# Optimization experiments

Hardware: AMD Instinct MI355X
Metric: run time of the kernel (lower is better)

## Reference

```python
import jax, jax.numpy as jnp
import numpy as np

N_HEADS = 16

def setup_inputs() -> dict:
    key = jax.random.key(0)
    ks = jax.random.split(key, 4)
    B, T, C = 2, 2048, 1024
    scale = 0.02
    return {
        "x": jax.random.normal(ks[0], (B, T, C), dtype=jnp.float32),
        "w_qkv": jax.random.normal(ks[1], (C, 3 * C), dtype=jnp.float32) * scale,
        "b_qkv": jnp.zeros((3 * C,), dtype=jnp.float32),
        "w_out": jax.random.normal(ks[2], (C, C), dtype=jnp.float32) * scale,
        "b_out": jnp.zeros((C,), dtype=jnp.float32),
    }

def reference(x, w_qkv, b_qkv, w_out, b_out):
    B, T, C = x.shape
    H = N_HEADS
    hd = C // H
    qkv = x @ w_qkv + b_qkv                      # [B,T,3C]
    q, k, v = jnp.split(qkv, 3, axis=-1)
    # [B,H,T,hd]
    q = q.reshape(B, T, H, hd).transpose(0, 2, 1, 3)
    k = k.reshape(B, T, H, hd).transpose(0, 2, 1, 3)
    v = v.reshape(B, T, H, hd).transpose(0, 2, 1, 3)
    att = jnp.einsum('bhqd,bhkd->bhqk', q, k) / jnp.sqrt(jnp.float32(hd))
    causal = jnp.tril(jnp.ones((T, T), dtype=bool))
    att = jnp.where(causal, att, -jnp.inf)
    att = jax.nn.softmax(att, axis=-1)
    # dropout is identity in eval mode (p effectively 0 for reference)
    y = jnp.einsum('bhqk,bhkd->bhqd', att, v)
    y = y.transpose(0, 2, 1, 3).reshape(B, T, C)
    return y @ w_out + b_out
```

## Files before the change

### kernel.cpp

```cpp
#include <hip/hip_runtime.h>
#include <hip/hip_bf16.h>

#define DEVI __device__ __forceinline__

typedef __attribute__((ext_vector_type(8))) short bf16x8_t;
typedef __attribute__((ext_vector_type(4))) float f32x4_t;
typedef __attribute__((ext_vector_type(4))) short s16x4_t;
typedef __attribute__((ext_vector_type(2))) unsigned int u32x2_t;

#define QSCALE 0.18033688011112043f
#define EXP2F(x) __builtin_amdgcn_exp2f(x)

static DEVI unsigned short f2b_bits(float f) {
    unsigned int u = __float_as_uint(f);
    unsigned int r = (u + 0x7fffu + ((u >> 16) & 1u)) >> 16;
    return (unsigned short)r;
}

static DEVI unsigned int cvtpk_bf16(float lo, float hi) {
    unsigned int r;
    asm("v_cvt_pk_bf16_f32 %0, %1, %2" : "=v"(r) : "v"(lo), "v"(hi));
    return r;
}

static DEVI void gload16(const short* g, short* l) {
    __builtin_amdgcn_global_load_lds((const __attribute__((address_space(1))) void*)g,
                                     (__attribute__((address_space(3))) void*)l, 16, 0, 0);
}

__global__ void cast_bf16_k(const float* __restrict__ in, short* __restrict__ out, long n) {
    long i = ((long)blockIdx.x * blockDim.x + threadIdx.x) * 4;
    if (i >= n) return;
    const float4 v = *(const float4*)(in + i);
    s16x4_t o;
    o[0] = (short)f2b_bits(v.x); o[1] = (short)f2b_bits(v.y);
    o[2] = (short)f2b_bits(v.z); o[3] = (short)f2b_bits(v.w);
    *(s16x4_t*)(out + i) = o;
}

__global__ void transpose_cast(const float* __restrict__ w, short* __restrict__ wT,
                               int K, int N) {
    __shared__ float tile[32][33];
    const int n0 = blockIdx.x * 32, k0 = blockIdx.y * 32;
    const int tx = threadIdx.x, ty = threadIdx.y;
#pragma unroll
    for (int i = 0; i < 4; ++i)
        tile[ty + 8 * i][tx] = w[(long)(k0 + ty + 8 * i) * N + n0 + tx];
    __syncthreads();
#pragma unroll
    for (int i = 0; i < 4; ++i)
        wT[(long)(n0 + ty + 8 * i) * K + k0 + tx] = (short)f2b_bits(tile[tx][ty + 8 * i]);
}

template<int MODE>
__global__ __launch_bounds__(256, 2) void gemm_bt(const short* __restrict__ A,
                                                  const short* __restrict__ Bt,
                                                  const float* __restrict__ bias,
                                                  void* __restrict__ Cv,
                                                  short* __restrict__ vtp,
                                                  int M, int N, int K) {
    __shared__ __align__(16) short lsA[2][128 * 32];
    __shared__ __align__(16) short lsB[2][128 * 32];
    const int tid = threadIdx.x;
    const int lane = tid & 63;
    const int w = tid >> 6;
    const int wr = w >> 1, wc = w & 1;
    const int l15 = lane & 15, lg = lane >> 4;
    const long m0 = (long)blockIdx.y * 128;
    const long n0 = (long)blockIdx.x * 128;

    f32x4_t acc[4][4] = {};

    const int srow = tid >> 2;
    const int scol = (tid & 3) * 8;
    const short* gA = A + (m0 + srow) * (long)K + scol;
    const short* gB = Bt + (n0 + srow) * (long)K + scol;

    auto STAGE = [&](int kt, int bi) {
        gload16(gA + kt,                &lsA[bi][tid * 8]);
        gload16(gA + kt + (long)64 * K, &lsA[bi][tid * 8 + 2048]);
        gload16(gB + kt,                &lsB[bi][tid * 8]);
        gload16(gB + kt + (long)64 * K, &lsB[bi][tid * 8 + 2048]);
    };

    const int nt = K >> 5;
    STAGE(0, 0);
    __syncthreads();
    int buf = 0;

    for (int i = 0; i < nt; ++i) {
        if (i + 1 < nt) STAGE((i + 1) << 5, buf ^ 1);
        bf16x8_t af[4], bfr[4];
#pragma unroll
        for (int m = 0; m < 4; ++m)
            af[m] = *(const bf16x8_t*)&lsA[buf][(wr * 64 + m * 16 + l15) * 32 + lg * 8];
#pragma unroll
        for (int n = 0; n < 4; ++n)
            bfr[n] = *(const bf16x8_t*)&lsB[buf][(wc * 64 + n * 16 + l15) * 32 + lg * 8];
        __builtin_amdgcn_s_setprio(1);
#pragma unroll
        for (int m = 0; m < 4; ++m)
#pragma unroll
            for (int n = 0; n < 4; ++n)
                acc[m][n] = __builtin_amdgcn_mfma_f32_16x16x32_bf16(af[m], bfr[n], acc[m][n], 0, 0, 0);
        __builtin_amdgcn_s_setprio(0);
        __syncthreads();
        buf ^= 1;
    }

#pragma unroll
    for (int n = 0; n < 4; ++n) {
        const int col = (int)n0 + wc * 64 + n * 16 + l15;
        const float bv = bias[col];
        if (MODE == 1) {
#pragma unroll
            for (int m = 0; m < 4; ++m) {
                const long row = m0 + wr * 64 + m * 16 + lg * 4;
#pragma unroll
                for (int j = 0; j < 4; ++j)
                    ((float*)Cv)[(row + j) * N + col] = acc[m][n][j] + bv;
            }
        } else if (col < 2048) {
            const float sc = (col < 1024) ? QSCALE : 1.0f;
#pragma unroll
            for (int m = 0; m < 4; ++m) {
                const long row = m0 + wr * 64 + m * 16 + lg * 4;
#pragma unroll
                for (int j = 0; j < 4; ++j)
                    ((short*)Cv)[(row + j) * N + col] = (short)f2b_bits((acc[m][n][j] + bv) * sc);
            }
        } else {
            const int hc = col - 2048;
            const int hh = hc >> 6, dd = hc & 63;
#pragma unroll
            for (int m = 0; m < 4; ++m) {
                const long row = m0 + wr * 64 + m * 16 + lg * 4;
                const int bb = (int)(row >> 11), tt = (int)(row & 2047);
                s16x4_t pk;
#pragma unroll
                for (int j = 0; j < 4; ++j) pk[j] = (short)f2b_bits(acc[m][n][j] + bv);
                *(s16x4_t*)&vtp[((long)(bb * 16 + hh) * 64 + dd) * 2048 + tt] = pk;
            }
        }
    }
}

__global__ __launch_bounds__(256, 4) void attn_fwd(const short* __restrict__ qkv,
                                                   const short* __restrict__ vt,
                                                   short* __restrict__ y) {
    __shared__ __align__(16) short lsK[2][64 * 64];
    __shared__ __align__(16) short lsV[2][64 * 64];
    __shared__ __align__(16) short lsP[4 * 16 * 64];
    const int bid = blockIdx.x;
    const int bh = bid & 31;
    const int t = bid >> 5;
    const int qi = (t < 16) ? t : 47 - t;
    const int b = bh >> 4, h = bh & 15;
    const int tid = threadIdx.x, w = tid >> 6, lane = tid & 63;
    const int l15 = lane & 15, lg = lane >> 4;
    const int lg4 = lg * 4;
    const int swz = (l15 & 7) << 4;

    const long qrow = (long)qi * 64 + w * 16 + l15;
    const bf16x8_t qf0 = *(const bf16x8_t*)&qkv[((long)b * 2048 + qrow) * 3072 + h * 64 + lg * 8];
    const bf16x8_t qf1 = *(const bf16x8_t*)&qkv[((long)b * 2048 + qrow) * 3072 + h * 64 + 32 + lg * 8];

    const int srow = tid >> 3;
    const int scolb = (tid & 7) * 16;
    const int sc = (scolb ^ ((srow & 7) << 4)) >> 1;
    const short* gK = qkv + ((long)b * 2048 + srow) * 3072 + 1024 + h * 64 + sc;
    const short* gV = vt + ((long)bh * 64 + srow) * 2048 + sc;

    auto STAGE = [&](int jt, int bufi) {
        const short* k0 = gK + (long)jt * 64 * 3072;
        const short* v0 = gV + (long)jt * 64;
        gload16(k0,             &lsK[bufi][tid * 8]);
        gload16(k0 + 32 * 3072, &lsK[bufi][tid * 8 + 2048]);
        gload16(v0,             &lsV[bufi][tid * 8]);
        gload16(v0 + 32 * 2048, &lsV[bufi][tid * 8 + 2048]);
    };

    float mrow = -3e38f, lrow = 0.f;
    f32x4_t oacc[4] = {};

    STAGE(0, 0);
    __syncthreads();
    int buf = 0;

    for (int j = 0; j <= qi; ++j) {
        if (j < qi) STAGE(j + 1, buf ^ 1);
        const bool diag = (j == qi);
        const char* Kb = (const char*)lsK[buf];
        const char* Vb = (const char*)lsV[buf];

        f32x4_t s[4] = {};
        const int nlim = diag ? (w + 1) : 4;
        __builtin_amdgcn_s_setprio(1);
#pragma unroll
        for (int kq = 0; kq < 2; ++kq) {
            const bf16x8_t qf = kq ? qf1 : qf0;
#pragma unroll
            for (int n = 0; n < 4; ++n) {
                if (n < nlim) {
                    bf16x8_t kf = *(const bf16x8_t*)(Kb + (n * 16 + l15) * 128 + ((kq * 64 + lg * 16) ^ swz));
                    s[n] = __builtin_amdgcn_mfma_f32_16x16x32_bf16(kf, qf, s[n], 0, 0, 0);
                }
            }
        }
        __builtin_amdgcn_s_setprio(0);

        float p[4][4];
#pragma unroll
        for (int n = 0; n < 4; ++n)
#pragma unroll
            for (int r = 0; r < 4; ++r) p[n][r] = s[n][r];

        if (diag) {
            const int ql = w * 16 + l15 - lg4;
#pragma unroll
            for (int n = 0; n < 4; ++n)
#pragma unroll
                for (int r = 0; r < 4; ++r)
                    if (n * 16 + r > ql) p[n][r] = -3e38f;
        }

        float pm = -3e38f;
#pragma unroll
        for (int n = 0; n < 4; ++n)
            pm = fmaxf(pm, fmaxf(fmaxf(p[n][0], p[n][1]), fmaxf(p[n][2], p[n][3])));
        pm = fmaxf(pm, __shfl_xor(pm, 16));
        pm = fmaxf(pm, __shfl_xor(pm, 32));

        if (!__all(pm <= mrow + 8.f)) {
            const float mnew = fmaxf(mrow, pm);
            const float al = EXP2F(mrow - mnew);
            mrow = mnew;
            lrow *= al;
            float ar[4];
#pragma unroll
            for (int r = 0; r < 4; ++r) ar[r] = __shfl(al, lg4 + r);
#pragma unroll
            for (int n = 0; n < 4; ++n)
#pragma unroll
                for (int r = 0; r < 4; ++r) oacc[n][r] *= ar[r];
        }

        float lsum = 0.f;
        char* Pb = (char*)lsP + w * 2048 + l15 * 128;
#pragma unroll
        for (int n = 0; n < 4; ++n) {
#pragma unroll
            for (int r = 0; r < 4; ++r) {
                p[n][r] = EXP2F(p[n][r] - mrow);
                lsum += p[n][r];
            }
            u32x2_t dw;
            dw[0] = cvtpk_bf16(p[n][0], p[n][1]);
            dw[1] = cvtpk_bf16(p[n][2], p[n][3]);
            *(u32x2_t*)(Pb + ((n * 32 + lg * 8) ^ swz)) = dw;
        }
        lsum += __shfl_xor(lsum, 16);
        lsum += __shfl_xor(lsum, 32);
        lrow += lsum;

        asm volatile("s_waitcnt lgkmcnt(0)" ::: "memory");

        __builtin_amdgcn_s_setprio(1);
#pragma unroll
        for (int kk = 0; kk < 2; ++kk) {
            if (!(diag && kk * 32 > w * 16 + 15)) {
                bf16x8_t pf = *(const bf16x8_t*)(Pb + ((kk * 64 + lg * 16) ^ swz));
#pragma unroll
                for (int n = 0; n < 4; ++n) {
                    bf16x8_t vf = *(const bf16x8_t*)(Vb + (n * 16 + l15) * 128 + ((kk * 64 + lg * 16) ^ swz));
                    oacc[n] = __builtin_amdgcn_mfma_f32_16x16x32_bf16(pf, vf, oacc[n], 0, 0, 0);
                }
            }
        }
        __builtin_amdgcn_s_setprio(0);
        __syncthreads();
        buf ^= 1;
    }

    float lr[4];
#pragma unroll
    for (int r = 0; r < 4; ++r) lr[r] = 1.0f / __shfl(lrow, lg4 + r);
#pragma unroll
    for (int n = 0; n < 4; ++n)
#pragma unroll
        for (int r = 0; r < 4; ++r) {
            const float ov = oacc[n][r] * lr[r];
            y[((long)b * 2048 + qi * 64 + w * 16 + lg4 + r) * 1024 + h * 64 + n * 16 + l15] =
                (short)f2b_bits(ov);
        }
}

extern "C" void kernel_launch(void* const* d_in, const int* in_sizes, int n_in,
                              void* d_out, int out_size, void* d_ws, size_t ws_size,
                              hipStream_t stream) {
    const float* x     = (const float*)d_in[0];
    const float* w_qkv = (const float*)d_in[1];
    const float* b_qkv = (const float*)d_in[2];
    const float* w_out = (const float*)d_in[3];
    const float* b_out = (const float*)d_in[4];

    char* ws = (char*)d_ws;
    size_t off = 0;
    short* xb    = (short*)(ws + off); off += (size_t)4096 * 1024 * 2;
    short* wqkvT = (short*)(ws + off); off += (size_t)3072 * 1024 * 2;
    short* woutT = (short*)(ws + off); off += (size_t)1024 * 1024 * 2;
    short* qkvb  = (short*)(ws + off); off += (size_t)4096 * 3072 * 2;
    short* vt    = (short*)(ws + off); off += (size_t)32 * 64 * 2048 * 2;
    short* yatt  = (short*)(ws + off); off += (size_t)4096 * 1024 * 2;

    cast_bf16_k<<<4096, 256, 0, stream>>>(x, xb, 4194304L);
    transpose_cast<<<dim3(96, 32), dim3(32, 8), 0, stream>>>(w_qkv, wqkvT, 1024, 3072);
    transpose_cast<<<dim3(32, 32), dim3(32, 8), 0, stream>>>(w_out, woutT, 1024, 1024);
    gemm_bt<0><<<dim3(24, 32), 256, 0, stream>>>(xb, wqkvT, b_qkv, (void*)qkvb, vt, 4096, 3072, 1024);
    attn_fwd<<<1024, 256, 0, stream>>>(qkvb, vt, yatt);
    gemm_bt<1><<<dim3(8, 32), 256, 0, stream>>>(yatt, woutT, b_out, d_out, nullptr, 4096, 1024, 1024);
}
```

Measured before the change: 188.3 us.

## Fuse prep kernels, narrow output GEMM tile, use split vmcnt barriers

Merges the x cast and the two weight transpose-casts into one launch to cut launch overhead. Replaces __syncthreads with explicit s_waitcnt vmcnt plus s_barrier in both the GEMM and attention loops, so the next stage's loads stay in flight while the current buffer is consumed. Templates the GEMM on N-fragment count so the output projection uses 128x64 tiles and twice as many blocks for better CU fill, and raises launch bounds to 3 blocks per CU. It also drops the setprio hints in the GEMM. The hand-counted vmcnt values must match the number of issued loads or the kernels will read stale shared memory.

```diff
diff --git a/kernel.cpp b/kernel.cpp
--- a/kernel.cpp
+++ b/kernel.cpp
@@ -28,21 +28,33 @@
                                      (__attribute__((address_space(3))) void*)l, 16, 0, 0);
 }
 
-__global__ void cast_bf16_k(const float* __restrict__ in, short* __restrict__ out, long n) {
-    long i = ((long)blockIdx.x * blockDim.x + threadIdx.x) * 4;
-    if (i >= n) return;
-    const float4 v = *(const float4*)(in + i);
-    s16x4_t o;
-    o[0] = (short)f2b_bits(v.x); o[1] = (short)f2b_bits(v.y);
-    o[2] = (short)f2b_bits(v.z); o[3] = (short)f2b_bits(v.w);
-    *(s16x4_t*)(out + i) = o;
-}
-
-__global__ void transpose_cast(const float* __restrict__ w, short* __restrict__ wT,
-                               int K, int N) {
+#define MEMFENCE asm volatile("" ::: "memory")
+
+__global__ __launch_bounds__(256) void prep_k(const float* __restrict__ x, short* __restrict__ xb,
+                                              const float* __restrict__ wqkv, short* __restrict__ wqkvT,
+                                              const float* __restrict__ wout, short* __restrict__ woutT) {
+    const int bid = blockIdx.x;
+    const int tid = threadIdx.x;
+    if (bid < 4096) {
+        const long i = ((long)bid * 256 + tid) * 4;
+        const float4 v = *(const float4*)(x + i);
+        s16x4_t o;
+        o[0] = (short)f2b_bits(v.x); o[1] = (short)f2b_bits(v.y);
+        o[2] = (short)f2b_bits(v.z); o[3] = (short)f2b_bits(v.w);
+        *(s16x4_t*)(xb + i) = o;
+        return;
+    }
     __shared__ float tile[32][33];
-    const int n0 = blockIdx.x * 32, k0 = blockIdx.y * 32;
-    const int tx = threadIdx.x, ty = threadIdx.y;
+    const float* w; short* wT; int K, N, bx, by;
+    if (bid < 4096 + 3072) {
+        const int rel = bid - 4096;
+        w = wqkv; wT = wqkvT; K = 1024; N = 3072; bx = rel % 96; by = rel / 96;
+    } else {
+        const int rel = bid - 7168;
+        w = wout; wT = woutT; K = 1024; N = 1024; bx = rel & 31; by = rel >> 5;
+    }
+    const int n0 = bx * 32, k0 = by * 32;
+    const int tx = tid & 31, ty = tid >> 5;
 #pragma unroll
     for (int i = 0; i < 4; ++i)
         tile[ty + 8 * i][tx] = w[(long)(k0 + ty + 8 * i) * N + n0 + tx];
@@ -52,24 +64,24 @@
         wT[(long)(n0 + ty + 8 * i) * K + k0 + tx] = (short)f2b_bits(tile[tx][ty + 8 * i]);
 }
 
-template<int MODE>
-__global__ __launch_bounds__(256, 2) void gemm_bt(const short* __restrict__ A,
+template<int MODE, int NF>
+__global__ __launch_bounds__(256, 3) void gemm_bt(const short* __restrict__ A,
                                                   const short* __restrict__ Bt,
                                                   const float* __restrict__ bias,
                                                   void* __restrict__ Cv,
                                                   short* __restrict__ vtp,
                                                   int M, int N, int K) {
     __shared__ __align__(16) short lsA[2][128 * 32];
-    __shared__ __align__(16) short lsB[2][128 * 32];
+    __shared__ __align__(16) short lsB[2][32 * NF * 32];
     const int tid = threadIdx.x;
     const int lane = tid & 63;
     const int w = tid >> 6;
     const int wr = w >> 1, wc = w & 1;
     const int l15 = lane & 15, lg = lane >> 4;
     const long m0 = (long)blockIdx.y * 128;
-    const long n0 = (long)blockIdx.x * 128;
-
-    f32x4_t acc[4][4] = {};
+    const long n0 = (long)blockIdx.x * (32 * NF);
+
+    f32x4_t acc[4][NF] = {};
 
     const int srow = tid >> 2;
     const int scol = (tid & 3) * 8;
@@ -80,37 +92,43 @@
         gload16(gA + kt,                &lsA[bi][tid * 8]);
         gload16(gA + kt + (long)64 * K, &lsA[bi][tid * 8 + 2048]);
         gload16(gB + kt,                &lsB[bi][tid * 8]);
-        gload16(gB + kt + (long)64 * K, &lsB[bi][tid * 8 + 2048]);
+        if (NF == 4) gload16(gB + kt + (long)64 * K, &lsB[bi][tid * 8 + 2048]);
     };
 
     const int nt = K >> 5;
     STAGE(0, 0);
-    __syncthreads();
     int buf = 0;
 
     for (int i = 0; i < nt; ++i) {
-        if (i + 1 < nt) STAGE((i + 1) << 5, buf ^ 1);
-        bf16x8_t af[4], bfr[4];
+        if (i + 1 < nt) {
+            STAGE((i + 1) << 5, buf ^ 1);
+            if (NF == 4) asm volatile("s_waitcnt vmcnt(4)" ::: "memory");
+            else         asm volatile("s_waitcnt vmcnt(3)" ::: "memory");
+        } else {
+            asm volatile("s_waitcnt vmcnt(0)" ::: "memory");
+        }
+        __builtin_amdgcn_s_barrier();
+        MEMFENCE;
+        bf16x8_t af[4], bfr[NF];
 #pragma unroll
         for (int m = 0; m < 4; ++m)
             af[m] = *(const bf16x8_t*)&lsA[buf][(wr * 64 + m * 16 + l15) * 32 + lg * 8];
 #pragma unroll
-        for (int n = 0; n < 4; ++n)
-            bfr[n] = *(const bf16x8_t*)&lsB[buf][(wc * 64 + n * 16 + l15) * 32 + lg * 8];
-        __builtin_amdgcn_s_setprio(1);
+        for (int n = 0; n < NF; ++n)
+            bfr[n] = *(const bf16x8_t*)&lsB[buf][(wc * NF * 16 + n * 16 + l15) * 32 + lg * 8];
 #pragma unroll
         for (int m = 0; m < 4; ++m)
 #pragma unroll
-            for (int n = 0; n < 4; ++n)
+            for (int n = 0; n < NF; ++n)
                 acc[m][n] = __builtin_amdgcn_mfma_f32_16x16x32_bf16(af[m], bfr[n], acc[m][n], 0, 0, 0);
-        __builtin_amdgcn_s_setprio(0);
-        __syncthreads();
+        MEMFENCE;
+        __builtin_amdgcn_s_barrier();
         buf ^= 1;
     }
 
 #pragma unroll
-    for (int n = 0; n < 4; ++n) {
-        const int col = (int)n0 + wc * 64 + n * 16 + l15;
+    for (int n = 0; n < NF; ++n) {
+        const int col = (int)n0 + wc * NF * 16 + n * 16 + l15;
         const float bv = bias[col];
         if (MODE == 1) {
 #pragma unroll
@@ -184,11 +202,18 @@
     f32x4_t oacc[4] = {};
 
     STAGE(0, 0);
-    __syncthreads();
     int buf = 0;
 
     for (int j = 0; j <= qi; ++j) {
-        if (j < qi) STAGE(j + 1, buf ^ 1);
+        if (j < qi) {
+            STAGE(j + 1, buf ^ 1);
+            asm volatile("s_waitcnt vmcnt(4)" ::: "memory");
+        } else {
+            asm volatile("s_waitcnt vmcnt(0)" ::: "memory");
+        }
+        __builtin_amdgcn_s_barrier();
+        MEMFENCE;
+
         const bool diag = (j == qi);
         const char* Kb = (const char*)lsK[buf];
         const char* Vb = (const char*)lsV[buf];
@@ -278,7 +303,8 @@
             }
         }
         __builtin_amdgcn_s_setprio(0);
-        __syncthreads();
+        MEMFENCE;
+        __builtin_amdgcn_s_barrier();
         buf ^= 1;
     }
 
@@ -313,10 +339,8 @@
     short* vt    = (short*)(ws + off); off += (size_t)32 * 64 * 2048 * 2;
     short* yatt  = (short*)(ws + off); off += (size_t)4096 * 1024 * 2;
 
-    cast_bf16_k<<<4096, 256, 0, stream>>>(x, xb, 4194304L);
-    transpose_cast<<<dim3(96, 32), dim3(32, 8), 0, stream>>>(w_qkv, wqkvT, 1024, 3072);
-    transpose_cast<<<dim3(32, 32), dim3(32, 8), 0, stream>>>(w_out, woutT, 1024, 1024);
-    gemm_bt<0><<<dim3(24, 32), 256, 0, stream>>>(xb, wqkvT, b_qkv, (void*)qkvb, vt, 4096, 3072, 1024);
+    prep_k<<<8192, 256, 0, stream>>>(x, xb, w_qkv, wqkvT, w_out, woutT);
+    gemm_bt<0, 4><<<dim3(24, 32), 256, 0, stream>>>(xb, wqkvT, b_qkv, (void*)qkvb, vt, 4096, 3072, 1024);
     attn_fwd<<<1024, 256, 0, stream>>>(qkvb, vt, yatt);
-    gemm_bt<1><<<dim3(8, 32), 256, 0, stream>>>(yatt, woutT, b_out, d_out, nullptr, 4096, 1024, 1024);
-}
+    gemm_bt<1, 2><<<dim3(16, 32), 256, 0, stream>>>(yatt, woutT, b_out, d_out, nullptr, 4096, 1024, 1024);
+}
```

After: 179.4 us. 1.05x faster.
